# Performance work log

Hardware: AMD Instinct MI355X
Metric: run time of the kernel (lower is better)

Reference implementation:

```python
import jax, jax.numpy as jnp
import numpy as np

N, V = 256, 128000
TEMPERATURE = 1.0
TOP_P = 0.9


def setup_inputs() -> dict:
    key = jax.random.key(0)
    k1, k2 = jax.random.split(key)
    logits = jax.random.normal(k1, (N, V), dtype=jnp.float32) * 4.0
    u = jax.random.uniform(k2, (N, V), dtype=jnp.float32, minval=1e-9, maxval=1.0)
    gumbel = -jnp.log(-jnp.log(u))  # Gumbel(0,1) noise for categorical sampling
    return {"logits": logits, "gumbel": gumbel, "top_k": 50}


def reference(logits, gumbel, top_k):
    fmin = jnp.finfo(logits.dtype).min
    # sanitize non-finite logits (matches torch.where(isfinite, ...))
    logits = jnp.where(jnp.isfinite(logits), logits, fmin)
    # temperature > 0 path
    logits = logits / TEMPERATURE
    # ---- top-p (nucleus) filtering ----
    sort_idx = jnp.argsort(-logits, axis=-1)                     # descending order indices [N,V]
    sorted_logits = jnp.take_along_axis(logits, sort_idx, axis=-1)
    cum_probs = jnp.cumsum(jax.nn.softmax(sorted_logits, axis=-1), axis=-1)
    remove_sorted = cum_probs > TOP_P
    # shift right by one; always keep the top-1 token
    remove_sorted = jnp.concatenate(
        [jnp.zeros_like(remove_sorted[..., :1]), remove_sorted[..., :-1]], axis=-1)
    # scatter mask back to original order via inverse permutation
    inv_perm = jnp.argsort(sort_idx, axis=-1)
    mask = jnp.take_along_axis(remove_sorted, inv_perm, axis=-1)
    logits = jnp.where(mask, fmin, logits)
    # ---- top-k filtering ----
    kth = jax.lax.top_k(logits, top_k)[0][..., -1:]              # k-th largest per row
    logits = jnp.where(logits < kth, fmin, logits)
    # ---- softmax + categorical sample (Gumbel-max trick) ----
    probs = jax.nn.softmax(logits, axis=-1)
    x0 = jnp.argmax(logits + gumbel, axis=-1)                    # ~ Categorical(probs)
    initial_confidence = jnp.take_along_axis(probs, x0[..., None], axis=-1)[..., 0]
    confidence = initial_confidence
    return confidence, x0.astype(jnp.int32), initial_confidence
```

## Files before the change

### kernel.cpp

```cpp
#include <hip/hip_runtime.h>
#include <cstdint>
#include <cfloat>
#include <math.h>

#define VCAB 128000
#define NROWS 256
#define NTHREADS 1024
#define NBUCK 8192
#define CAP 1024

__device__ __forceinline__ unsigned mono(float f) {
    unsigned u = __float_as_uint(f);
    return (u & 0x80000000u) ? ~u : (u | 0x80000000u);
}
__device__ __forceinline__ float unmono(unsigned k) {
    return __uint_as_float((k & 0x80000000u) ? (k ^ 0x80000000u) : ~k);
}

__global__ __launch_bounds__(NTHREADS) void sampler_kernel(
    const float* __restrict__ logits,
    const float* __restrict__ gumbel,
    const int* __restrict__ topk_p,
    float* __restrict__ out)
{
    const int row = blockIdx.x;
    const int t = threadIdx.x;
    const size_t base = (size_t)row * VCAB;
    const float4* rowv = reinterpret_cast<const float4*>(logits + base);
    const float FMIN = -FLT_MAX;

    __shared__ unsigned hist[NBUCK];
    __shared__ unsigned chunkSum[NTHREADS];
    __shared__ unsigned sufs[NTHREADS];
    __shared__ unsigned long long ck[CAP];
    __shared__ unsigned candCnt;
    __shared__ unsigned sh_bstar;
    __shared__ float red[16];
    __shared__ float sh_m0, sh_S;

    #pragma unroll
    for (int j = 0; j < NBUCK / NTHREADS; ++j) hist[t + j * NTHREADS] = 0u;
    if (t == 0) { candCnt = 0u; sh_bstar = 0u; }
    __syncthreads();

    float lmax = FMIN;
    for (int i = t; i < VCAB / 4; i += NTHREADS) {
        float4 x = rowv[i];
        float vs[4] = {x.x, x.y, x.z, x.w};
        #pragma unroll
        for (int c = 0; c < 4; ++c) {
            float v = vs[c];
            if (!(fabsf(v) <= FLT_MAX)) v = FMIN;
            lmax = fmaxf(lmax, v);
            atomicAdd(&hist[mono(v) >> 19], 1u);
        }
    }
    for (int off = 32; off > 0; off >>= 1) lmax = fmaxf(lmax, __shfl_xor(lmax, off, 64));
    if ((t & 63) == 0) red[t >> 6] = lmax;
    __syncthreads();
    if (t < 16) {
        float m = red[t];
        for (int off = 8; off > 0; off >>= 1) m = fmaxf(m, __shfl_xor(m, off, 16));
        if (t == 0) sh_m0 = m;
    }
    __syncthreads();
    const float m0 = sh_m0;

    unsigned cs = 0;
    #pragma unroll
    for (int j = 0; j < NBUCK / NTHREADS; ++j) cs += hist[t * (NBUCK / NTHREADS) + j];
    chunkSum[t] = cs;
    sufs[t] = cs;
    __syncthreads();
    for (int off = 1; off < NTHREADS; off <<= 1) {
        unsigned add = (t + off < NTHREADS) ? sufs[t + off] : 0u;
        __syncthreads();
        sufs[t] += add;
        __syncthreads();
    }
    {
        unsigned incl = sufs[t];
        unsigned above = incl - cs;
        if (incl >= 64u && above < 64u) {
            unsigned acc = above;
            const int bpc = NBUCK / NTHREADS;
            for (int b = t * bpc + bpc - 1; b >= t * bpc; --b) {
                acc += hist[b];
                if (acc >= 64u) { sh_bstar = (unsigned)b; break; }
            }
        }
    }
    __syncthreads();
    const unsigned bstar = sh_bstar;

    ck[t] = 0ull;
    __syncthreads();

    float ssum = 0.f;
    for (int i = t; i < VCAB / 4; i += NTHREADS) {
        float4 x = rowv[i];
        float vs[4] = {x.x, x.y, x.z, x.w};
        #pragma unroll
        for (int c = 0; c < 4; ++c) {
            float v = vs[c];
            if (!(fabsf(v) <= FLT_MAX)) v = FMIN;
            ssum += expf(v - m0);
            unsigned k = mono(v);
            if ((k >> 19) >= bstar) {
                unsigned pos = atomicAdd(&candCnt, 1u);
                if (pos < CAP)
                    ck[pos] = ((unsigned long long)k << 32) |
                              (unsigned long long)(~(unsigned)(i * 4 + c));
            }
        }
    }
    for (int off = 32; off > 0; off >>= 1) ssum += __shfl_xor(ssum, off, 64);
    if ((t & 63) == 0) red[t >> 6] = ssum;
    __syncthreads();
    if (t < 16) {
        float s = red[t];
        for (int off = 8; off > 0; off >>= 1) s += __shfl_xor(s, off, 16);
        if (t == 0) sh_S = s;
    }
    __syncthreads();
    const float S = sh_S;

    for (unsigned k = 2; k <= CAP; k <<= 1) {
        for (unsigned j = k >> 1; j > 0; j >>= 1) {
            __syncthreads();
            unsigned l = (unsigned)t ^ j;
            if (l > (unsigned)t) {
                unsigned long long a = ck[t], b = ck[l];
                bool up = (((unsigned)t & k) == 0u);
                if (up ? (a < b) : (a > b)) { ck[t] = b; ck[l] = a; }
            }
        }
    }
    __syncthreads();

    if (t < 64) {
        unsigned long long key = ck[t];
        float v = unmono((unsigned)(key >> 32));
        int idx = (int)(~(unsigned)key);
        int K = *topk_p;
        K = min(max(K, 1), 64);

        float p = expf(v - m0) / S;
        float pref = p;
        for (int off = 1; off < 64; off <<= 1) {
            float xx = __shfl_up(pref, off, 64);
            if (t >= off) pref += xx;
        }
        float Eex = pref - p;
        int M = (int)__popcll(__ballot(Eex <= 0.9f));

        int Mfinal;
        if (M >= K) {
            float kth = __shfl(v, K - 1, 64);
            int J = (int)__popcll(__ballot(v >= kth));
            Mfinal = min(M, J);
        } else {
            Mfinal = M;
        }

        bool act = (t < Mfinal);
        float g  = act ? gumbel[base + (size_t)idx] : 0.f;
        float tt = act ? (v + g) : -FLT_MAX;
        int   ti = act ? idx : 0x7FFFFFFF;
        float bv = v;
        float bt = tt; int bi = ti;
        for (int off = 32; off > 0; off >>= 1) {
            float ot = __shfl_xor(bt, off, 64);
            int   oi = __shfl_xor(bi, off, 64);
            float ov = __shfl_xor(bv, off, 64);
            if (ot > bt || (ot == bt && oi < bi)) { bt = ot; bi = oi; bv = ov; }
        }
        float e = act ? expf(v - m0) : 0.f;
        float Z = e;
        for (int off = 32; off > 0; off >>= 1) Z += __shfl_xor(Z, off, 64);

        if (t == 0) {
            float conf = expf(bv - m0) / Z;
            out[row] = conf;
            out[NROWS + row] = (float)bi;
            out[2 * NROWS + row] = conf;
        }
    }
}

extern "C" void kernel_launch(void* const* d_in, const int* in_sizes, int n_in,
                              void* d_out, int out_size, void* d_ws, size_t ws_size,
                              hipStream_t stream) {
    const float* logits = (const float*)d_in[0];
    const float* gumbel = (const float*)d_in[1];
    const int*   topk   = (const int*)d_in[2];
    float* out = (float*)d_out;
    sampler_kernel<<<NROWS, NTHREADS, 0, stream>>>(logits, gumbel, topk, out);
}
```

Baseline: 277.5 us.

## Fold max, softmax sum and candidate collection into one pass via sampled threshold

Builds a histogram from an 8K-element sample to pick a conservative candidate threshold, then does a single full pass that computes the max, the exp-sum (shifted by the sample max), and collects candidates above the threshold into a buffer. A wave-level histogram walk replaces the block-wide suffix scan, and the candidate buffer is refined by a second histogram rather than a second full read of the row. The bitonic sort shrinks to 256 elements when few candidates remain. A fallback third pass over the row handles candidate overflow. Using the sample max as the exp shift risks overflow if the true max is far above it.

```diff
diff --git a/kernel.cpp b/kernel.cpp
--- a/kernel.cpp
+++ b/kernel.cpp
@@ -5,9 +5,10 @@
 
 #define VCAB 128000
 #define NROWS 256
-#define NTHREADS 1024
+#define NTH 1024
 #define NBUCK 8192
-#define CAP 1024
+#define CAP2 2560
+#define CKN 1024
 
 __device__ __forceinline__ unsigned mono(float f) {
     unsigned u = __float_as_uint(f);
@@ -17,7 +18,32 @@
     return __uint_as_float((k & 0x80000000u) ? (k ^ 0x80000000u) : ~k);
 }
 
-__global__ __launch_bounds__(NTHREADS) void sampler_kernel(
+__device__ __forceinline__ unsigned find_bstar_wave(const unsigned* hist, int startb, int lane) {
+    int hb = startb;
+    unsigned cum = 0u;
+    for (int it = 0; it < 200; ++it) {
+        int b = hb - lane;
+        unsigned c = (b >= 0 && b < NBUCK) ? hist[b] : 0u;
+        unsigned p = c;
+        #pragma unroll
+        for (int off = 1; off < 64; off <<= 1) {
+            unsigned q = __shfl_up(p, off, 64);
+            if (lane >= off) p += q;
+        }
+        unsigned long long mm = __ballot(cum + p >= 64u);
+        if (mm) {
+            int l = __builtin_ctzll(mm);
+            int b2 = hb - l;
+            return (unsigned)(b2 > 0 ? b2 : 0);
+        }
+        cum += __shfl(p, 63, 64);
+        hb -= 64;
+        if (hb < 0) return 0u;
+    }
+    return 0u;
+}
+
+__global__ __launch_bounds__(NTH) void sampler_kernel(
     const float* __restrict__ logits,
     const float* __restrict__ gumbel,
     const int* __restrict__ topk_p,
@@ -27,112 +53,146 @@
     const int t = threadIdx.x;
     const size_t base = (size_t)row * VCAB;
     const float4* rowv = reinterpret_cast<const float4*>(logits + base);
-    const float FMIN = -FLT_MAX;
 
     __shared__ unsigned hist[NBUCK];
-    __shared__ unsigned chunkSum[NTHREADS];
-    __shared__ unsigned sufs[NTHREADS];
-    __shared__ unsigned long long ck[CAP];
-    __shared__ unsigned candCnt;
-    __shared__ unsigned sh_bstar;
-    __shared__ float red[16];
-    __shared__ float sh_m0, sh_S;
+    __shared__ unsigned long long cand[CAP2];
+    __shared__ unsigned long long ck[CKN];
+    __shared__ unsigned candCnt, candCnt2;
+    __shared__ unsigned sh_bsamp, sh_bfin;
+    __shared__ float red[16], red2[16];
+    __shared__ float sh_msamp, sh_m0, sh_S;
 
     #pragma unroll
-    for (int j = 0; j < NBUCK / NTHREADS; ++j) hist[t + j * NTHREADS] = 0u;
-    if (t == 0) { candCnt = 0u; sh_bstar = 0u; }
-    __syncthreads();
-
-    float lmax = FMIN;
-    for (int i = t; i < VCAB / 4; i += NTHREADS) {
+    for (int j = 0; j < NBUCK / NTH; ++j) hist[t + j * NTH] = 0u;
+    if (t == 0) { candCnt = 0u; candCnt2 = 0u; }
+    __syncthreads();
+
+    float smax = -FLT_MAX;
+    #pragma unroll
+    for (int ii = 0; ii < 2; ++ii) {
+        float4 x = rowv[t + ii * NTH];
+        float vs[4] = {x.x, x.y, x.z, x.w};
+        #pragma unroll
+        for (int c = 0; c < 4; ++c) {
+            float v = vs[c];
+            if (!(fabsf(v) <= FLT_MAX)) v = -FLT_MAX;
+            smax = fmaxf(smax, v);
+            atomicAdd(&hist[mono(v) >> 19], 1u);
+        }
+    }
+    for (int off = 32; off > 0; off >>= 1) smax = fmaxf(smax, __shfl_xor(smax, off, 64));
+    if ((t & 63) == 0) red[t >> 6] = smax;
+    __syncthreads();
+    if (t < 16) {
+        float m = red[t];
+        #pragma unroll
+        for (int off = 8; off > 0; off >>= 1) m = fmaxf(m, __shfl_xor(m, off, 16));
+        if (t == 0) sh_msamp = m;
+    }
+    __syncthreads();
+    const float msamp = sh_msamp;
+
+    if (t < 64) {
+        unsigned b = find_bstar_wave(hist, (int)(mono(msamp) >> 19), t);
+        if (t == 0) sh_bsamp = b;
+    }
+    __syncthreads();
+    const float thrV = unmono(sh_bsamp << 19);
+    #pragma unroll
+    for (int j = 0; j < NBUCK / NTH; ++j) hist[t + j * NTH] = 0u;
+    __syncthreads();
+
+    float sacc[4] = {0.f, 0.f, 0.f, 0.f};
+    float lacc[4] = {-FLT_MAX, -FLT_MAX, -FLT_MAX, -FLT_MAX};
+    for (int i = t; i < VCAB / 4; i += NTH) {
         float4 x = rowv[i];
         float vs[4] = {x.x, x.y, x.z, x.w};
         #pragma unroll
         for (int c = 0; c < 4; ++c) {
             float v = vs[c];
-            if (!(fabsf(v) <= FLT_MAX)) v = FMIN;
-            lmax = fmaxf(lmax, v);
-            atomicAdd(&hist[mono(v) >> 19], 1u);
-        }
-    }
-    for (int off = 32; off > 0; off >>= 1) lmax = fmaxf(lmax, __shfl_xor(lmax, off, 64));
-    if ((t & 63) == 0) red[t >> 6] = lmax;
+            if (!(fabsf(v) <= FLT_MAX)) v = -FLT_MAX;
+            lacc[c] = fmaxf(lacc[c], v);
+            sacc[c] += __expf(v - msamp);
+            if (v >= thrV) {
+                unsigned k = mono(v);
+                atomicAdd(&hist[k >> 19], 1u);
+                unsigned pos = atomicAdd(&candCnt, 1u);
+                if (pos < CAP2)
+                    cand[pos] = ((unsigned long long)k << 32) |
+                                (unsigned long long)(~(unsigned)(i * 4 + c));
+            }
+        }
+    }
+    float s = (sacc[0] + sacc[1]) + (sacc[2] + sacc[3]);
+    float lmax = fmaxf(fmaxf(lacc[0], lacc[1]), fmaxf(lacc[2], lacc[3]));
+    for (int off = 32; off > 0; off >>= 1) {
+        lmax = fmaxf(lmax, __shfl_xor(lmax, off, 64));
+        s += __shfl_xor(s, off, 64);
+    }
+    if ((t & 63) == 0) { red[t >> 6] = lmax; red2[t >> 6] = s; }
     __syncthreads();
     if (t < 16) {
-        float m = red[t];
-        for (int off = 8; off > 0; off >>= 1) m = fmaxf(m, __shfl_xor(m, off, 16));
-        if (t == 0) sh_m0 = m;
-    }
-    __syncthreads();
-    const float m0 = sh_m0;
-
-    unsigned cs = 0;
-    #pragma unroll
-    for (int j = 0; j < NBUCK / NTHREADS; ++j) cs += hist[t * (NBUCK / NTHREADS) + j];
-    chunkSum[t] = cs;
-    sufs[t] = cs;
-    __syncthreads();
-    for (int off = 1; off < NTHREADS; off <<= 1) {
-        unsigned add = (t + off < NTHREADS) ? sufs[t + off] : 0u;
-        __syncthreads();
-        sufs[t] += add;
-        __syncthreads();
-    }
-    {
-        unsigned incl = sufs[t];
-        unsigned above = incl - cs;
-        if (incl >= 64u && above < 64u) {
-            unsigned acc = above;
-            const int bpc = NBUCK / NTHREADS;
-            for (int b = t * bpc + bpc - 1; b >= t * bpc; --b) {
-                acc += hist[b];
-                if (acc >= 64u) { sh_bstar = (unsigned)b; break; }
-            }
-        }
-    }
-    __syncthreads();
-    const unsigned bstar = sh_bstar;
+        float m = red[t], z = red2[t];
+        #pragma unroll
+        for (int off = 8; off > 0; off >>= 1) {
+            m = fmaxf(m, __shfl_xor(m, off, 16));
+            z += __shfl_xor(z, off, 16);
+        }
+        if (t == 0) { sh_m0 = m; sh_S = z; }
+    }
+    __syncthreads();
+    const float S = sh_S;
+
+    if (t < 64) {
+        unsigned b = find_bstar_wave(hist, (int)(mono(sh_m0) >> 19), t);
+        if (t == 0) sh_bfin = b;
+    }
+    __syncthreads();
+    const unsigned bfin = sh_bfin;
 
     ck[t] = 0ull;
     __syncthreads();
-
-    float ssum = 0.f;
-    for (int i = t; i < VCAB / 4; i += NTHREADS) {
-        float4 x = rowv[i];
-        float vs[4] = {x.x, x.y, x.z, x.w};
-        #pragma unroll
-        for (int c = 0; c < 4; ++c) {
-            float v = vs[c];
-            if (!(fabsf(v) <= FLT_MAX)) v = FMIN;
-            ssum += expf(v - m0);
-            unsigned k = mono(v);
-            if ((k >> 19) >= bstar) {
-                unsigned pos = atomicAdd(&candCnt, 1u);
-                if (pos < CAP)
-                    ck[pos] = ((unsigned long long)k << 32) |
-                              (unsigned long long)(~(unsigned)(i * 4 + c));
-            }
-        }
-    }
-    for (int off = 32; off > 0; off >>= 1) ssum += __shfl_xor(ssum, off, 64);
-    if ((t & 63) == 0) red[t >> 6] = ssum;
-    __syncthreads();
-    if (t < 16) {
-        float s = red[t];
-        for (int off = 8; off > 0; off >>= 1) s += __shfl_xor(s, off, 16);
-        if (t == 0) sh_S = s;
-    }
-    __syncthreads();
-    const float S = sh_S;
-
-    for (unsigned k = 2; k <= CAP; k <<= 1) {
-        for (unsigned j = k >> 1; j > 0; j >>= 1) {
+    if (candCnt <= CAP2) {
+        const unsigned nc = candCnt;
+        for (unsigned j = t; j < nc; j += NTH) {
+            unsigned long long e = cand[j];
+            if ((unsigned)(e >> 51) >= bfin) {
+                unsigned pos = atomicAdd(&candCnt2, 1u);
+                if (pos < CKN) ck[pos] = e;
+            }
+        }
+    } else {
+        const float thr2 = unmono(bfin << 19);
+        for (int i = t; i < VCAB / 4; i += NTH) {
+            float4 x = rowv[i];
+            float vs[4] = {x.x, x.y, x.z, x.w};
+            #pragma unroll
+            for (int c = 0; c < 4; ++c) {
+                float v = vs[c];
+                if (!(fabsf(v) <= FLT_MAX)) v = -FLT_MAX;
+                if (v >= thr2) {
+                    unsigned pos = atomicAdd(&candCnt2, 1u);
+                    if (pos < CKN)
+                        ck[pos] = ((unsigned long long)mono(v) << 32) |
+                                  (unsigned long long)(~(unsigned)(i * 4 + c));
+                }
+            }
+        }
+    }
+    __syncthreads();
+
+    const unsigned nc2 = candCnt2 < (unsigned)CKN ? candCnt2 : (unsigned)CKN;
+    const int nsort = (nc2 <= 256u) ? 256 : CKN;
+    for (int k = 2; k <= nsort; k <<= 1) {
+        for (int j = k >> 1; j > 0; j >>= 1) {
             __syncthreads();
-            unsigned l = (unsigned)t ^ j;
-            if (l > (unsigned)t) {
-                unsigned long long a = ck[t], b = ck[l];
-                bool up = (((unsigned)t & k) == 0u);
-                if (up ? (a < b) : (a > b)) { ck[t] = b; ck[l] = a; }
+            if (t < nsort) {
+                int l = t ^ j;
+                if (l > t) {
+                    unsigned long long a = ck[t], b = ck[l];
+                    bool up = ((t & k) == 0);
+                    if (up ? (a < b) : (a > b)) { ck[t] = b; ck[l] = a; }
+                }
             }
         }
     }
@@ -145,7 +205,7 @@
         int K = *topk_p;
         K = min(max(K, 1), 64);
 
-        float p = expf(v - m0) / S;
+        float p = expf(v - msamp) / S;
         float pref = p;
         for (int off = 1; off < 64; off <<= 1) {
             float xx = __shfl_up(pref, off, 64);
@@ -175,12 +235,12 @@
             float ov = __shfl_xor(bv, off, 64);
             if (ot > bt || (ot == bt && oi < bi)) { bt = ot; bi = oi; bv = ov; }
         }
-        float e = act ? expf(v - m0) : 0.f;
+        float e = act ? expf(v - msamp) : 0.f;
         float Z = e;
         for (int off = 32; off > 0; off >>= 1) Z += __shfl_xor(Z, off, 64);
 
         if (t == 0) {
-            float conf = expf(bv - m0) / Z;
+            float conf = expf(bv - msamp) / Z;
             out[row] = conf;
             out[NROWS + row] = (float)bi;
             out[2 * NROWS + row] = conf;
@@ -195,5 +255,5 @@
     const float* gumbel = (const float*)d_in[1];
     const int*   topk   = (const int*)d_in[2];
     float* out = (float*)d_out;
-    sampler_kernel<<<NROWS, NTHREADS, 0, stream>>>(logits, gumbel, topk, out);
-}
+    sampler_kernel<<<NROWS, NTH, 0, stream>>>(logits, gumbel, topk, out);
+}
```

Result: faster. 252.5 us (-9.0%).
